# Performance work log

Hardware: AMD Instinct MI355X
Metric: run time of the kernel (lower is better)

Reference implementation:

```python
import jax, jax.numpy as jnp
import numpy as np

# Config (matches init_kwargs)
N, A, H, W = 4, 16, 384, 384
B_SIZE = 8      # block_size per spatial dim
STRIDE = 4      # block_stride per spatial dim (overlapping blocks)
THRESH = 2.0    # singular-value soft threshold
NB = (H - B_SIZE) // STRIDE + 1   # blocks per spatial dim (95)
P = B_SIZE * B_SIZE               # pixels per block (64)


def _block_indices():
    """Flat pixel index for each (block, in-block pixel): [NB*NB, P] int32."""
    starts = np.arange(NB) * STRIDE
    ih = starts[:, None] + np.arange(B_SIZE)              # [NB, b] row coords
    flat = ih[:, None, :, None] * W + ih[None, :, None, :]  # [NBh, NBw, b, b]
    return flat.reshape(NB * NB, P).astype(np.int32)


def setup_inputs() -> dict:
    key = jax.random.key(0)
    x = jax.random.normal(key, (N, A, H, W), dtype=jnp.float32)
    idx = jnp.asarray(_block_indices())
    # precompute_normalization: overlap-add of ones -> per-pixel block count
    block_weights = jnp.zeros(H * W, jnp.float32).at[idx].add(1.0).reshape(H, W)
    return {"x": x, "block_weights": block_weights}


def reference(x, block_weights):
    idx = jnp.asarray(_block_indices())           # [B, P]
    # self.shift = (0, 0) on the first forward call -> rolls are identity
    x = jnp.roll(x, (0, 0), axis=(-2, -1))
    xf = x.reshape(N, A, H * W)
    blocks = xf[:, :, idx]                        # [N, A, B, P] block extraction
    m = jnp.transpose(blocks, (0, 2, 3, 1))       # 'n a b p -> n b p a' -> [N,B,P,A]
    U, S, Vh = jnp.linalg.svd(m, full_matrices=False)  # U:[N,B,P,A] S:[N,B,A] Vh:[N,B,A,A]
    S = jnp.maximum(S - THRESH, 0.0)              # soft-threshold singular values
    m = (U * S[..., None, :]) @ Vh                # U diag(S) Vh, [N,B,P,A]
    blocks = jnp.transpose(m, (0, 3, 1, 2))       # 'n b p a -> n a b p'
    # adjoint: overlap-add fold, then normalize by block counts
    out = jnp.zeros((N, A, H * W), x.dtype).at[:, :, idx].add(blocks)
    out = out.reshape(N, A, H, W) / block_weights
    return jnp.roll(out, (0, 0), axis=(-2, -1))
```

## Files before the change

kernel.cpp:

```cpp
#include <hip/hip_runtime.h>


typedef __attribute__((ext_vector_type(2))) float v2f;
typedef __attribute__((ext_vector_type(4))) float f32x4;
typedef __attribute__((ext_vector_type(8))) short s16x8;
typedef union { float4 f4; v2f v2[2]; } f4v2;

#define N_      4
#define A_      16
#define H_      384
#define W_      384
#define PLANE_  (H_*W_)
#define NB_     95
#define NBB_    (NB_*NB_)
#define NMAT_   (N_*NBB_)
#define NWAVE_  ((NMAT_ + 3) / 4)
#define NSWEEP_ 4
#define PHI_BYTES_ ((size_t)NMAT_ * 256 * 4)

__device__ __forceinline__ v2f pk_fma(v2f a, v2f b, v2f c) {
    v2f d; asm("v_pk_fma_f32 %0, %1, %2, %3" : "=v"(d) : "v"(a), "v"(b), "v"(c));
    return d;
}
__device__ __forceinline__ v2f pk_mul(v2f a, v2f b) {
    v2f d; asm("v_pk_mul_f32 %0, %1, %2" : "=v"(d) : "v"(a), "v"(b));
    return d;
}

__device__ __forceinline__ unsigned cvtpk_bf16(float a, float b) {
    unsigned d;
    asm("v_cvt_pk_bf16_f32 %0, %1, %2" : "=v"(d) : "v"(a), "v"(b));
    return d;
}
__device__ __forceinline__ float asf_(unsigned u) {
    union { unsigned u; float f; } x; x.u = u; return x.f;
}
typedef union { s16x8 s8; unsigned u[4]; } frag8;

__device__ __forceinline__ void split8(const float4 A, const float4 B,
                                       frag8& hi, frag8& lo) {
    hi.u[0] = cvtpk_bf16(A.x, A.y);
    hi.u[1] = cvtpk_bf16(A.z, A.w);
    hi.u[2] = cvtpk_bf16(B.x, B.y);
    hi.u[3] = cvtpk_bf16(B.z, B.w);
    const float l0 = A.x - asf_(hi.u[0] << 16);
    const float l1 = A.y - asf_(hi.u[0] & 0xFFFF0000u);
    const float l2 = A.z - asf_(hi.u[1] << 16);
    const float l3 = A.w - asf_(hi.u[1] & 0xFFFF0000u);
    const float l4 = B.x - asf_(hi.u[2] << 16);
    const float l5 = B.y - asf_(hi.u[2] & 0xFFFF0000u);
    const float l6 = B.z - asf_(hi.u[3] << 16);
    const float l7 = B.w - asf_(hi.u[3] & 0xFFFF0000u);
    lo.u[0] = cvtpk_bf16(l0, l1);
    lo.u[1] = cvtpk_bf16(l2, l3);
    lo.u[2] = cvtpk_bf16(l4, l5);
    lo.u[3] = cvtpk_bf16(l6, l7);
}

template<int CTRL>
__device__ __forceinline__ float dpp16(float v) {
    union { float f; int i; } u; u.f = v;
    u.i = __builtin_amdgcn_mov_dpp(u.i, CTRL, 0xF, 0xF, true);
    return u.f;
}

#define QP1_ 0xB1
#define QP2_ 0x4E
#define QP3_ 0x1B
#define HM_  0x141
#define FM_  0x140
#define R8_  0x128

template<int M>
__device__ __forceinline__ float lane_xor16(float v) {
    if constexpr (M == 1)       return dpp16<QP1_>(v);
    else if constexpr (M == 2)  return dpp16<QP2_>(v);
    else if constexpr (M == 3)  return dpp16<QP3_>(v);
    else if constexpr (M == 7)  return dpp16<HM_>(v);
    else if constexpr (M == 8)  return dpp16<R8_>(v);
    else if constexpr (M == 15) return dpp16<FM_>(v);
    else {
        union { float f; int i; } u; u.f = v;
        u.i = __builtin_amdgcn_ds_swizzle(u.i, (M << 10) | 0x1F);
        return u.f;
    }
}

template<int M>
__device__ __forceinline__ void jacobi_round(v2f w[8], float& nrm, const int j) {
    v2f pw[8];
    #pragma unroll
    for (int i = 0; i < 8; ++i) {
        pw[i][0] = lane_xor16<M>(w[i][0]);
        pw[i][1] = lane_xor16<M>(w[i][1]);
    }
    const float pn = lane_xor16<M>(nrm);

    v2f d0 = w[0]*pw[0], d1 = w[1]*pw[1];
    #pragma unroll
    for (int i = 2; i < 8; i += 2) {
        d0 = __builtin_elementwise_fma(w[i],   pw[i],   d0);
        d1 = __builtin_elementwise_fma(w[i+1], pw[i+1], d1);
    }
    const v2f ds = d0 + d1;
    const float gam = ds[0] + ds[1];

    const bool  low = ((j ^ M) > j);
    const float na  = low ? nrm : pn;
    const float nb  = low ? pn  : nrm;

    const float thr = 1e-12f * (na + nb);
    const bool  rot = fabsf(gam) > thr;
    const float gs  = rot ? gam : 1.f;
    const float zeta = (nb - na) * (0.5f * __builtin_amdgcn_rcpf(gs));
    const float rt   = __builtin_amdgcn_rcpf(
                           fabsf(zeta) +
                           __builtin_amdgcn_sqrtf(__builtin_fmaf(zeta, zeta, 1.f)));
    float t  = copysignf(rt, zeta);
    float c  = __builtin_amdgcn_rsqf(__builtin_fmaf(t, t, 1.f));
    float sv = c * t;
    if (!rot) { c = 1.f; sv = 0.f; t = 0.f; }

    const float ss = low ? -sv : sv;
    const v2f c2 = {c, c}, sp = {ss, ss};
    #pragma unroll
    for (int i = 0; i < 8; ++i)
        w[i] = __builtin_elementwise_fma(c2, w[i], sp*pw[i]);

    nrm = __builtin_fmaf(low ? -t : t, gam, nrm);
}

__device__ __forceinline__ void gram_jacobi_phi(
        const float* __restrict__ x, const int wid, const int warp,
        const int lane, float Gl[4][4][320]) {
    const int g   = lane >> 4;
    const int j   = lane & 15;
    const int kq4 = g * 4;

    #pragma unroll
    for (int s = 0; s < 4; ++s) {
        const int id  = wid * 4 + s;
        const int n   = id / NBB_;
        const int rem = id % NBB_;
        const int bi  = rem / NB_;
        const int bj  = rem % NB_;
        const float* bp = x + (size_t)n * (A_ * PLANE_) + (size_t)j * PLANE_
                            + (bi*4 + g) * W_ + bj*4;

        const float4 va = *(const float4*)(bp);
        const float4 vb = *(const float4*)(bp + 4);
        const float4 vc = *(const float4*)(bp + 4*W_);
        const float4 vd = *(const float4*)(bp + 4*W_ + 4);

        frag8 hi0, lo0, hi1, lo1;
        split8(va, vb, hi0, lo0);
        split8(vc, vd, hi1, lo1);

        f32x4 C = {0.f, 0.f, 0.f, 0.f};
        C = __builtin_amdgcn_mfma_f32_16x16x32_bf16(lo0.s8, hi0.s8, C, 0, 0, 0);
        C = __builtin_amdgcn_mfma_f32_16x16x32_bf16(hi0.s8, lo0.s8, C, 0, 0, 0);
        C = __builtin_amdgcn_mfma_f32_16x16x32_bf16(hi0.s8, hi0.s8, C, 0, 0, 0);
        C = __builtin_amdgcn_mfma_f32_16x16x32_bf16(lo1.s8, hi1.s8, C, 0, 0, 0);
        C = __builtin_amdgcn_mfma_f32_16x16x32_bf16(hi1.s8, lo1.s8, C, 0, 0, 0);
        C = __builtin_amdgcn_mfma_f32_16x16x32_bf16(hi1.s8, hi1.s8, C, 0, 0, 0);

        *(float4*)&Gl[warp][s][j*20 + kq4] = make_float4(C[0], C[1], C[2], C[3]);
    }
    __builtin_amdgcn_wave_barrier();

    v2f w[8];
    {
        f4v2 t0, t1, t2, t3;
        t0.f4 = *(const float4*)&Gl[warp][g][j*20 + 0];
        t1.f4 = *(const float4*)&Gl[warp][g][j*20 + 4];
        t2.f4 = *(const float4*)&Gl[warp][g][j*20 + 8];
        t3.f4 = *(const float4*)&Gl[warp][g][j*20 + 12];
        w[0]=t0.v2[0]; w[1]=t0.v2[1]; w[2]=t1.v2[0]; w[3]=t1.v2[1];
        w[4]=t2.v2[0]; w[5]=t2.v2[1]; w[6]=t3.v2[0]; w[7]=t3.v2[1];
    }
    float nrm;
    {
        v2f d = pk_mul(w[0], w[0]);
        #pragma unroll
        for (int i = 1; i < 8; ++i) d = pk_fma(w[i], w[i], d);
        nrm = d[0] + d[1];
    }

    for (int sweep = 0; sweep < NSWEEP_; ++sweep) {
        jacobi_round<1>(w, nrm, j);  jacobi_round<2>(w, nrm, j);
        jacobi_round<3>(w, nrm, j);  jacobi_round<4>(w, nrm, j);
        jacobi_round<5>(w, nrm, j);  jacobi_round<6>(w, nrm, j);
        jacobi_round<7>(w, nrm, j);  jacobi_round<8>(w, nrm, j);
        jacobi_round<9>(w, nrm, j);  jacobi_round<10>(w, nrm, j);
        jacobi_round<11>(w, nrm, j); jacobi_round<12>(w, nrm, j);
        jacobi_round<13>(w, nrm, j); jacobi_round<14>(w, nrm, j);
        jacobi_round<15>(w, nrm, j);
    }
    {
        v2f d = pk_mul(w[0], w[0]);
        #pragma unroll
        for (int i = 1; i < 8; ++i) d = pk_fma(w[i], w[i], d);
        nrm = d[0] + d[1];
    }
    float rho = 0.f;
    if (nrm > 16.f) {
        const float lam = __builtin_amdgcn_sqrtf(nrm);
        rho = (1.f - 2.f * __builtin_amdgcn_rsqf(lam)) * __builtin_amdgcn_rcpf(nrm);
    }

    __builtin_amdgcn_wave_barrier();
    *(float4*)&Gl[warp][g][j*20 + 0]  = make_float4(w[0][0], w[0][1], w[1][0], w[1][1]);
    *(float4*)&Gl[warp][g][j*20 + 4]  = make_float4(w[2][0], w[2][1], w[3][0], w[3][1]);
    *(float4*)&Gl[warp][g][j*20 + 8]  = make_float4(w[4][0], w[4][1], w[5][0], w[5][1]);
    *(float4*)&Gl[warp][g][j*20 + 12] = make_float4(w[6][0], w[6][1], w[7][0], w[7][1]);
    Gl[warp][g][j*20 + 16] = rho;
    __builtin_amdgcn_wave_barrier();

    {
        const int kg = lane >> 4;
        const int mn = lane & 15;
        f32x4 PhiC[4];
        #pragma unroll
        for (int s = 0; s < 4; ++s) {
            frag8 Ahi, Alo, Bhi, Blo;
            if (kg < 2) {
                float av[8], bv[8];
                #pragma unroll
                for (int e = 0; e < 8; ++e) {
                    const int k = kg*8 + e;
                    const float wv = Gl[warp][s][k*20 + mn];
                    const float rh = Gl[warp][s][k*20 + 16];
                    bv[e] = wv;
                    av[e] = wv * rh;
                }
                split8(make_float4(av[0],av[1],av[2],av[3]),
                       make_float4(av[4],av[5],av[6],av[7]), Ahi, Alo);
                split8(make_float4(bv[0],bv[1],bv[2],bv[3]),
                       make_float4(bv[4],bv[5],bv[6],bv[7]), Bhi, Blo);
            } else {
                Ahi.u[0]=0u; Ahi.u[1]=0u; Ahi.u[2]=0u; Ahi.u[3]=0u;
                Alo = Ahi; Bhi = Ahi; Blo = Ahi;
            }
            f32x4 C = {0.f, 0.f, 0.f, 0.f};
            C = __builtin_amdgcn_mfma_f32_16x16x32_bf16(Alo.s8, Bhi.s8, C, 0, 0, 0);
            C = __builtin_amdgcn_mfma_f32_16x16x32_bf16(Ahi.s8, Blo.s8, C, 0, 0, 0);
            C = __builtin_amdgcn_mfma_f32_16x16x32_bf16(Ahi.s8, Bhi.s8, C, 0, 0, 0);
            PhiC[s] = C;
        }
        __builtin_amdgcn_wave_barrier();
        #pragma unroll
        for (int s = 0; s < 4; ++s) {
            #pragma unroll
            for (int r2 = 0; r2 < 4; ++r2)
                Gl[warp][s][(4*kg + r2)*20 + mn] = PhiC[s][r2];
        }
        __builtin_amdgcn_wave_barrier();
    }
}

__global__ __launch_bounds__(256, 8)
void llr_phi(const float* __restrict__ x, float* __restrict__ phiG) {
    __shared__ __align__(16) float Gl[4][4][320];
    const int warp = threadIdx.x >> 6;
    const int lane = threadIdx.x & 63;

    const int xcd = blockIdx.x & 7, idx = blockIdx.x >> 3;
    const int wg  = (xcd == 0 ? idx : 283 + (xcd - 1) * 282 + idx);
    const int wid = wg * 4 + warp;
    if (wid >= NWAVE_) return;

    gram_jacobi_phi(x, wid, warp, lane, Gl);

    const int g = lane >> 4, j = lane & 15;
    float* pb = phiG + (size_t)(wid*4 + g) * 256 + j * 16;
    const float4 p0 = *(const float4*)&Gl[warp][g][j*20 + 0];
    const float4 p1 = *(const float4*)&Gl[warp][g][j*20 + 4];
    const float4 p2 = *(const float4*)&Gl[warp][g][j*20 + 8];
    const float4 p3 = *(const float4*)&Gl[warp][g][j*20 + 12];
    *(float4*)&pb[0]  = p0;  *(float4*)&pb[4]  = p1;
    *(float4*)&pb[8]  = p2;  *(float4*)&pb[12] = p3;
}

__global__ __launch_bounds__(256, 8)
void llr_out2(const float* __restrict__ x, const float* __restrict__ phiG,
              float* __restrict__ out) {
    __shared__ __align__(16) float Sl[16][260];

    const int b  = (blockIdx.x & 7) * 288 + (blockIdx.x >> 3);
    const int n  = b / 576;
    const int tt = b % 576;
    const int tr = tt / 12, tc = tt % 12;
    const int r0 = tr*8, c0 = tc*32;
    const int cr0 = tr*2, cc0 = tc*8;

    const int r = threadIdx.x >> 5;
    const int c = threadIdx.x & 31;
    const int lcc = ((r >> 2) << 3) + (c >> 2);
    const size_t sb = (size_t)n * (A_*PLANE_) + (size_t)(r0 + r) * W_ + (c0 + c);

    {
        const int lc = threadIdx.x >> 4;
        const int fo = (threadIdx.x & 15) * 4;
        const int ci = cr0 + (lc >> 3);
        const int cj = cc0 + (lc & 7);
        const int bi0 = max(ci - 1, 0), bi1 = min(ci, NB_ - 1);
        const int bj0 = max(cj - 1, 0), bj1 = min(cj, NB_ - 1);
        const size_t r00 = ((size_t)(n*NBB_ + bi0*NB_ + bj0))*256;
        const size_t r01 = ((size_t)(n*NBB_ + bi0*NB_ + bj1))*256;
        const size_t r10 = ((size_t)(n*NBB_ + bi1*NB_ + bj0))*256;
        const size_t r11 = ((size_t)(n*NBB_ + bi1*NB_ + bj1))*256;
        #pragma unroll
        for (int it = 0; it < 4; ++it) {
            const int off = fo + it*64;
            const float4 a  = *(const float4*)&phiG[r00 + off];
            const float4 bq = *(const float4*)&phiG[r01 + off];
            const float4 cq = *(const float4*)&phiG[r10 + off];
            const float4 d  = *(const float4*)&phiG[r11 + off];
            float4 s;
            s.x = (a.x + bq.x + cq.x + d.x) * 0.25f;
            s.y = (a.y + bq.y + cq.y + d.y) * 0.25f;
            s.z = (a.z + bq.z + cq.z + d.z) * 0.25f;
            s.w = (a.w + bq.w + cq.w + d.w) * 0.25f;
            *(float4*)&Sl[lc][off] = s;
        }
    }

    float xk[16];
    #pragma unroll
    for (int k = 0; k < 16; ++k) xk[k] = x[sb + (size_t)k * PLANE_];

    __syncthreads();

    v2f acc[8];
    #pragma unroll
    for (int i = 0; i < 8; ++i) acc[i] = (v2f){0.f, 0.f};
    #pragma unroll
    for (int k = 0; k < 16; ++k) {
        const v2f xv = {xk[k], xk[k]};
        f4v2 s0, s1, s2, s3;
        s0.f4 = *(const float4*)&Sl[lcc][k*16 + 0];
        s1.f4 = *(const float4*)&Sl[lcc][k*16 + 4];
        s2.f4 = *(const float4*)&Sl[lcc][k*16 + 8];
        s3.f4 = *(const float4*)&Sl[lcc][k*16 + 12];
        acc[0] = pk_fma(xv, s0.v2[0], acc[0]);
        acc[1] = pk_fma(xv, s0.v2[1], acc[1]);
        acc[2] = pk_fma(xv, s1.v2[0], acc[2]);
        acc[3] = pk_fma(xv, s1.v2[1], acc[3]);
        acc[4] = pk_fma(xv, s2.v2[0], acc[4]);
        acc[5] = pk_fma(xv, s2.v2[1], acc[5]);
        acc[6] = pk_fma(xv, s3.v2[0], acc[6]);
        acc[7] = pk_fma(xv, s3.v2[1], acc[7]);
    }
    #pragma unroll
    for (int i = 0; i < 8; ++i) {
        out[sb + (size_t)(2*i)     * PLANE_] = acc[i][0];
        out[sb + (size_t)(2*i + 1) * PLANE_] = acc[i][1];
    }
}

__global__ __launch_bounds__(256, 5)
void llr_fused(const float* __restrict__ x, float* __restrict__ out) {
    __shared__ __align__(16) float Gl[4][4][320];
    const int warp = threadIdx.x >> 6;
    const int lane = threadIdx.x & 63;
    const int wid  = blockIdx.x * 4 + warp;
    if (wid >= NWAVE_) return;

    gram_jacobi_phi(x, wid, warp, lane, Gl);

    const int pr = lane >> 3, pc = lane & 7;
    for (int s = 0; s < 4; ++s) {
        const int id = wid*4 + s;
        const int n = id / NBB_, rem = id % NBB_;
        const int bi = rem / NB_, bj = rem % NB_;
        const int base = n*(A_*PLANE_) + (bi*4+pr)*W_ + (bj*4+pc);
        float mr[16];
        #pragma unroll
        for (int a = 0; a < 16; ++a) mr[a] = x[base + a*PLANE_];
        float o[16];
        #pragma unroll
        for (int a = 0; a < 16; ++a) o[a] = 0.f;
        #pragma unroll
        for (int k = 0; k < 16; ++k) {
            const float mk = mr[k];
            const float4 f0 = *(const float4*)&Gl[warp][s][k*20 + 0];
            const float4 f1 = *(const float4*)&Gl[warp][s][k*20 + 4];
            const float4 f2 = *(const float4*)&Gl[warp][s][k*20 + 8];
            const float4 f3 = *(const float4*)&Gl[warp][s][k*20 + 12];
            o[0]+=mk*f0.x;  o[1]+=mk*f0.y;  o[2]+=mk*f0.z;  o[3]+=mk*f0.w;
            o[4]+=mk*f1.x;  o[5]+=mk*f1.y;  o[6]+=mk*f1.z;  o[7]+=mk*f1.w;
            o[8]+=mk*f2.x;  o[9]+=mk*f2.y;  o[10]+=mk*f2.z; o[11]+=mk*f2.w;
            o[12]+=mk*f3.x; o[13]+=mk*f3.y; o[14]+=mk*f3.z; o[15]+=mk*f3.w;
        }
        #pragma unroll
        for (int a = 0; a < 16; ++a)
            unsafeAtomicAdd(&out[base + a*PLANE_], o[a]);
    }
}

__global__ __launch_bounds__(256)
void llr_div(float* __restrict__ out, const float* __restrict__ bw) {
    const int i = (blockIdx.x * 256 + threadIdx.x) * 4;
    float4 o = *(float4*)&out[i];
    const float4 bv = *(const float4*)&bw[i % PLANE_];
    o.x /= bv.x; o.y /= bv.y; o.z /= bv.z; o.w /= bv.w;
    *(float4*)&out[i] = o;
}

extern "C" void kernel_launch(void* const* d_in, const int* in_sizes, int n_in,
                              void* d_out, int out_size, void* d_ws, size_t ws_size,
                              hipStream_t stream) {
    (void)in_sizes; (void)n_in;
    const float* x  = (const float*)d_in[0];
    const float* bw = (const float*)d_in[1];
    float* out = (float*)d_out;

    if (ws_size >= PHI_BYTES_) {
        float* phiG = (float*)d_ws;
        hipLaunchKernelGGL(llr_phi,  dim3((NWAVE_ + 3) / 4), dim3(256), 0, stream, x, phiG);
        hipLaunchKernelGGL(llr_out2, dim3(4 * 48 * 12),      dim3(256), 0, stream, x, phiG, out);
    } else {
        hipMemsetAsync(out, 0, (size_t)out_size * sizeof(float), stream);
        hipLaunchKernelGGL(llr_fused, dim3((NWAVE_ + 3) / 4), dim3(256), 0, stream, x, out);
        hipLaunchKernelGGL(llr_div, dim3((N_*A_*PLANE_) / (256*4)), dim3(256), 0, stream, out, bw);
    }
}
```

Before: 172.8 us.

## Process eight matrices per wave with two interleaved Jacobi chains

```diff
diff --git a/kernel.cpp b/kernel.cpp
--- a/kernel.cpp
+++ b/kernel.cpp
@@ -14,7 +14,7 @@
 #define NB_     95
 #define NBB_    (NB_*NB_)
 #define NMAT_   (N_*NBB_)
-#define NWAVE_  ((NMAT_ + 3) / 4)
+#define NWAVE8_ ((NMAT_ + 7) / 8)
 #define NSWEEP_ 4
 #define PHI_BYTES_ ((size_t)NMAT_ * 256 * 4)
 
@@ -87,141 +87,205 @@
 }
 
 template<int M>
-__device__ __forceinline__ void jacobi_round(v2f w[8], float& nrm, const int j) {
-    v2f pw[8];
+__device__ __forceinline__ void jacobi_round2(v2f wA[8], v2f wB[8],
+                                              float& nrmA, float& nrmB,
+                                              const int j) {
+    v2f pA[8], pB[8];
     #pragma unroll
     for (int i = 0; i < 8; ++i) {
-        pw[i][0] = lane_xor16<M>(w[i][0]);
-        pw[i][1] = lane_xor16<M>(w[i][1]);
-    }
-    const float pn = lane_xor16<M>(nrm);
-
-    v2f d0 = w[0]*pw[0], d1 = w[1]*pw[1];
+        pA[i][0] = lane_xor16<M>(wA[i][0]);
+        pA[i][1] = lane_xor16<M>(wA[i][1]);
+        pB[i][0] = lane_xor16<M>(wB[i][0]);
+        pB[i][1] = lane_xor16<M>(wB[i][1]);
+    }
+    const float pnA = lane_xor16<M>(nrmA);
+    const float pnB = lane_xor16<M>(nrmB);
+
+    v2f a0 = wA[0]*pA[0], a1 = wA[1]*pA[1];
+    v2f b0 = wB[0]*pB[0], b1 = wB[1]*pB[1];
     #pragma unroll
     for (int i = 2; i < 8; i += 2) {
-        d0 = __builtin_elementwise_fma(w[i],   pw[i],   d0);
-        d1 = __builtin_elementwise_fma(w[i+1], pw[i+1], d1);
-    }
-    const v2f ds = d0 + d1;
-    const float gam = ds[0] + ds[1];
-
-    const bool  low = ((j ^ M) > j);
-    const float na  = low ? nrm : pn;
-    const float nb  = low ? pn  : nrm;
-
-    const float thr = 1e-12f * (na + nb);
-    const bool  rot = fabsf(gam) > thr;
-    const float gs  = rot ? gam : 1.f;
-    const float zeta = (nb - na) * (0.5f * __builtin_amdgcn_rcpf(gs));
-    const float rt   = __builtin_amdgcn_rcpf(
-                           fabsf(zeta) +
-                           __builtin_amdgcn_sqrtf(__builtin_fmaf(zeta, zeta, 1.f)));
-    float t  = copysignf(rt, zeta);
-    float c  = __builtin_amdgcn_rsqf(__builtin_fmaf(t, t, 1.f));
-    float sv = c * t;
-    if (!rot) { c = 1.f; sv = 0.f; t = 0.f; }
-
-    const float ss = low ? -sv : sv;
-    const v2f c2 = {c, c}, sp = {ss, ss};
-    #pragma unroll
-    for (int i = 0; i < 8; ++i)
-        w[i] = __builtin_elementwise_fma(c2, w[i], sp*pw[i]);
-
-    nrm = __builtin_fmaf(low ? -t : t, gam, nrm);
+        a0 = __builtin_elementwise_fma(wA[i],   pA[i],   a0);
+        a1 = __builtin_elementwise_fma(wA[i+1], pA[i+1], a1);
+        b0 = __builtin_elementwise_fma(wB[i],   pB[i],   b0);
+        b1 = __builtin_elementwise_fma(wB[i+1], pB[i+1], b1);
+    }
+    const v2f dsA = a0 + a1;
+    const v2f dsB = b0 + b1;
+    const float gamA = dsA[0] + dsA[1];
+    const float gamB = dsB[0] + dsB[1];
+
+    const bool low = ((j ^ M) > j);
+
+    const float naA = low ? nrmA : pnA;
+    const float nbA = low ? pnA  : nrmA;
+    const float thrA = 1e-12f * (naA + nbA);
+    const bool  rotA = fabsf(gamA) > thrA;
+    const float gsA  = rotA ? gamA : 1.f;
+    const float zA = (nbA - naA) * (0.5f * __builtin_amdgcn_rcpf(gsA));
+    const float rtA = __builtin_amdgcn_rcpf(
+                          fabsf(zA) +
+                          __builtin_amdgcn_sqrtf(__builtin_fmaf(zA, zA, 1.f)));
+    float tA = copysignf(rtA, zA);
+    float cA = __builtin_amdgcn_rsqf(__builtin_fmaf(tA, tA, 1.f));
+    float svA = cA * tA;
+    if (!rotA) { cA = 1.f; svA = 0.f; tA = 0.f; }
+
+    const float naB = low ? nrmB : pnB;
+    const float nbB = low ? pnB  : nrmB;
+    const float thrB = 1e-12f * (naB + nbB);
+    const bool  rotB = fabsf(gamB) > thrB;
+    const float gsB  = rotB ? gamB : 1.f;
+    const float zB = (nbB - naB) * (0.5f * __builtin_amdgcn_rcpf(gsB));
+    const float rtB = __builtin_amdgcn_rcpf(
+                          fabsf(zB) +
+                          __builtin_amdgcn_sqrtf(__builtin_fmaf(zB, zB, 1.f)));
+    float tB = copysignf(rtB, zB);
+    float cB = __builtin_amdgcn_rsqf(__builtin_fmaf(tB, tB, 1.f));
+    float svB = cB * tB;
+    if (!rotB) { cB = 1.f; svB = 0.f; tB = 0.f; }
+
+    const float ssA = low ? -svA : svA;
+    const float ssB = low ? -svB : svB;
+    const v2f cA2 = {cA, cA}, sA2 = {ssA, ssA};
+    const v2f cB2 = {cB, cB}, sB2 = {ssB, ssB};
+    #pragma unroll
+    for (int i = 0; i < 8; ++i) {
+        wA[i] = __builtin_elementwise_fma(cA2, wA[i], sA2*pA[i]);
+        wB[i] = __builtin_elementwise_fma(cB2, wB[i], sB2*pB[i]);
+    }
+
+    nrmA = __builtin_fmaf(low ? -tA : tA, gamA, nrmA);
+    nrmB = __builtin_fmaf(low ? -tB : tB, gamB, nrmB);
 }
 
 __device__ __forceinline__ void gram_jacobi_phi(
         const float* __restrict__ x, const int wid, const int warp,
-        const int lane, float Gl[4][4][320]) {
+        const int lane, float Gl[4][8][320]) {
     const int g   = lane >> 4;
     const int j   = lane & 15;
     const int kq4 = g * 4;
 
     #pragma unroll
-    for (int s = 0; s < 4; ++s) {
-        const int id  = wid * 4 + s;
-        const int n   = id / NBB_;
-        const int rem = id % NBB_;
-        const int bi  = rem / NB_;
-        const int bj  = rem % NB_;
-        const float* bp = x + (size_t)n * (A_ * PLANE_) + (size_t)j * PLANE_
-                            + (bi*4 + g) * W_ + bj*4;
-
-        const float4 va = *(const float4*)(bp);
-        const float4 vb = *(const float4*)(bp + 4);
-        const float4 vc = *(const float4*)(bp + 4*W_);
-        const float4 vd = *(const float4*)(bp + 4*W_ + 4);
-
-        frag8 hi0, lo0, hi1, lo1;
-        split8(va, vb, hi0, lo0);
-        split8(vc, vd, hi1, lo1);
-
-        f32x4 C = {0.f, 0.f, 0.f, 0.f};
-        C = __builtin_amdgcn_mfma_f32_16x16x32_bf16(lo0.s8, hi0.s8, C, 0, 0, 0);
-        C = __builtin_amdgcn_mfma_f32_16x16x32_bf16(hi0.s8, lo0.s8, C, 0, 0, 0);
-        C = __builtin_amdgcn_mfma_f32_16x16x32_bf16(hi0.s8, hi0.s8, C, 0, 0, 0);
-        C = __builtin_amdgcn_mfma_f32_16x16x32_bf16(lo1.s8, hi1.s8, C, 0, 0, 0);
-        C = __builtin_amdgcn_mfma_f32_16x16x32_bf16(hi1.s8, lo1.s8, C, 0, 0, 0);
-        C = __builtin_amdgcn_mfma_f32_16x16x32_bf16(hi1.s8, hi1.s8, C, 0, 0, 0);
-
-        *(float4*)&Gl[warp][s][j*20 + kq4] = make_float4(C[0], C[1], C[2], C[3]);
+    for (int s = 0; s < 8; ++s) {
+        const int id = wid * 8 + s;
+        if (id < NMAT_) {
+            const int n   = id / NBB_;
+            const int rem = id % NBB_;
+            const int bi  = rem / NB_;
+            const int bj  = rem % NB_;
+            const float* bp = x + (size_t)n * (A_ * PLANE_) + (size_t)j * PLANE_
+                                + (bi*4 + g) * W_ + bj*4;
+
+            const float4 va = *(const float4*)(bp);
+            const float4 vb = *(const float4*)(bp + 4);
+            const float4 vc = *(const float4*)(bp + 4*W_);
+            const float4 vd = *(const float4*)(bp + 4*W_ + 4);
+
+            frag8 hi0, lo0, hi1, lo1;
+            split8(va, vb, hi0, lo0);
+            split8(vc, vd, hi1, lo1);
+
+            f32x4 C = {0.f, 0.f, 0.f, 0.f};
+            C = __builtin_amdgcn_mfma_f32_16x16x32_bf16(lo0.s8, hi0.s8, C, 0, 0, 0);
+            C = __builtin_amdgcn_mfma_f32_16x16x32_bf16(hi0.s8, lo0.s8, C, 0, 0, 0);
+            C = __builtin_amdgcn_mfma_f32_16x16x32_bf16(hi0.s8, hi0.s8, C, 0, 0, 0);
+            C = __builtin_amdgcn_mfma_f32_16x16x32_bf16(lo1.s8, hi1.s8, C, 0, 0, 0);
+            C = __builtin_amdgcn_mfma_f32_16x16x32_bf16(hi1.s8, lo1.s8, C, 0, 0, 0);
+            C = __builtin_amdgcn_mfma_f32_16x16x32_bf16(hi1.s8, hi1.s8, C, 0, 0, 0);
+
+            *(float4*)&Gl[warp][s][j*20 + kq4] = make_float4(C[0], C[1], C[2], C[3]);
+        } else {
+            *(float4*)&Gl[warp][s][j*20 + kq4] = make_float4(0.f, 0.f, 0.f, 0.f);
+        }
     }
     __builtin_amdgcn_wave_barrier();
 
-    v2f w[8];
+    v2f wA[8], wB[8];
     {
         f4v2 t0, t1, t2, t3;
         t0.f4 = *(const float4*)&Gl[warp][g][j*20 + 0];
         t1.f4 = *(const float4*)&Gl[warp][g][j*20 + 4];
         t2.f4 = *(const float4*)&Gl[warp][g][j*20 + 8];
         t3.f4 = *(const float4*)&Gl[warp][g][j*20 + 12];
-        w[0]=t0.v2[0]; w[1]=t0.v2[1]; w[2]=t1.v2[0]; w[3]=t1.v2[1];
-        w[4]=t2.v2[0]; w[5]=t2.v2[1]; w[6]=t3.v2[0]; w[7]=t3.v2[1];
-    }
-    float nrm;
+        wA[0]=t0.v2[0]; wA[1]=t0.v2[1]; wA[2]=t1.v2[0]; wA[3]=t1.v2[1];
+        wA[4]=t2.v2[0]; wA[5]=t2.v2[1]; wA[6]=t3.v2[0]; wA[7]=t3.v2[1];
+        t0.f4 = *(const float4*)&Gl[warp][g+4][j*20 + 0];
+        t1.f4 = *(const float4*)&Gl[warp][g+4][j*20 + 4];
+        t2.f4 = *(const float4*)&Gl[warp][g+4][j*20 + 8];
+        t3.f4 = *(const float4*)&Gl[warp][g+4][j*20 + 12];
+        wB[0]=t0.v2[0]; wB[1]=t0.v2[1]; wB[2]=t1.v2[0]; wB[3]=t1.v2[1];
+        wB[4]=t2.v2[0]; wB[5]=t2.v2[1]; wB[6]=t3.v2[0]; wB[7]=t3.v2[1];
+    }
+    float nrmA, nrmB;
     {
-        v2f d = pk_mul(w[0], w[0]);
-        #pragma unroll
-        for (int i = 1; i < 8; ++i) d = pk_fma(w[i], w[i], d);
-        nrm = d[0] + d[1];
+        v2f dA = pk_mul(wA[0], wA[0]);
+        v2f dB = pk_mul(wB[0], wB[0]);
+        #pragma unroll
+        for (int i = 1; i < 8; ++i) {
+            dA = pk_fma(wA[i], wA[i], dA);
+            dB = pk_fma(wB[i], wB[i], dB);
+        }
+        nrmA = dA[0] + dA[1];
+        nrmB = dB[0] + dB[1];
     }
 
     for (int sweep = 0; sweep < NSWEEP_; ++sweep) {
-        jacobi_round<1>(w, nrm, j);  jacobi_round<2>(w, nrm, j);
-        jacobi_round<3>(w, nrm, j);  jacobi_round<4>(w, nrm, j);
-        jacobi_round<5>(w, nrm, j);  jacobi_round<6>(w, nrm, j);
-        jacobi_round<7>(w, nrm, j);  jacobi_round<8>(w, nrm, j);
-        jacobi_round<9>(w, nrm, j);  jacobi_round<10>(w, nrm, j);
-        jacobi_round<11>(w, nrm, j); jacobi_round<12>(w, nrm, j);
-        jacobi_round<13>(w, nrm, j); jacobi_round<14>(w, nrm, j);
-        jacobi_round<15>(w, nrm, j);
+        jacobi_round2<1>(wA, wB, nrmA, nrmB, j);
+        jacobi_round2<2>(wA, wB, nrmA, nrmB, j);
+        jacobi_round2<3>(wA, wB, nrmA, nrmB, j);
+        jacobi_round2<4>(wA, wB, nrmA, nrmB, j);
+        jacobi_round2<5>(wA, wB, nrmA, nrmB, j);
+        jacobi_round2<6>(wA, wB, nrmA, nrmB, j);
+        jacobi_round2<7>(wA, wB, nrmA, nrmB, j);
+        jacobi_round2<8>(wA, wB, nrmA, nrmB, j);
+        jacobi_round2<9>(wA, wB, nrmA, nrmB, j);
+        jacobi_round2<10>(wA, wB, nrmA, nrmB, j);
+        jacobi_round2<11>(wA, wB, nrmA, nrmB, j);
+        jacobi_round2<12>(wA, wB, nrmA, nrmB, j);
+        jacobi_round2<13>(wA, wB, nrmA, nrmB, j);
+        jacobi_round2<14>(wA, wB, nrmA, nrmB, j);
+        jacobi_round2<15>(wA, wB, nrmA, nrmB, j);
     }
     {
-        v2f d = pk_mul(w[0], w[0]);
-        #pragma unroll
-        for (int i = 1; i < 8; ++i) d = pk_fma(w[i], w[i], d);
-        nrm = d[0] + d[1];
-    }
-    float rho = 0.f;
-    if (nrm > 16.f) {
-        const float lam = __builtin_amdgcn_sqrtf(nrm);
-        rho = (1.f - 2.f * __builtin_amdgcn_rsqf(lam)) * __builtin_amdgcn_rcpf(nrm);
+        v2f dA = pk_mul(wA[0], wA[0]);
+        v2f dB = pk_mul(wB[0], wB[0]);
+        #pragma unroll
+        for (int i = 1; i < 8; ++i) {
+            dA = pk_fma(wA[i], wA[i], dA);
+            dB = pk_fma(wB[i], wB[i], dB);
+        }
+        nrmA = dA[0] + dA[1];
+        nrmB = dB[0] + dB[1];
+    }
+    float rhoA = 0.f, rhoB = 0.f;
+    if (nrmA > 16.f) {
+        const float lam = __builtin_amdgcn_sqrtf(nrmA);
+        rhoA = (1.f - 2.f * __builtin_amdgcn_rsqf(lam)) * __builtin_amdgcn_rcpf(nrmA);
+    }
+    if (nrmB > 16.f) {
+        const float lam = __builtin_amdgcn_sqrtf(nrmB);
+        rhoB = (1.f - 2.f * __builtin_amdgcn_rsqf(lam)) * __builtin_amdgcn_rcpf(nrmB);
     }
 
     __builtin_amdgcn_wave_barrier();
-    *(float4*)&Gl[warp][g][j*20 + 0]  = make_float4(w[0][0], w[0][1], w[1][0], w[1][1]);
-    *(float4*)&Gl[warp][g][j*20 + 4]  = make_float4(w[2][0], w[2][1], w[3][0], w[3][1]);
-    *(float4*)&Gl[warp][g][j*20 + 8]  = make_float4(w[4][0], w[4][1], w[5][0], w[5][1]);
-    *(float4*)&Gl[warp][g][j*20 + 12] = make_float4(w[6][0], w[6][1], w[7][0], w[7][1]);
-    Gl[warp][g][j*20 + 16] = rho;
+    *(float4*)&Gl[warp][g][j*20 + 0]  = make_float4(wA[0][0], wA[0][1], wA[1][0], wA[1][1]);
+    *(float4*)&Gl[warp][g][j*20 + 4]  = make_float4(wA[2][0], wA[2][1], wA[3][0], wA[3][1]);
+    *(float4*)&Gl[warp][g][j*20 + 8]  = make_float4(wA[4][0], wA[4][1], wA[5][0], wA[5][1]);
+    *(float4*)&Gl[warp][g][j*20 + 12] = make_float4(wA[6][0], wA[6][1], wA[7][0], wA[7][1]);
+    Gl[warp][g][j*20 + 16] = rhoA;
+    *(float4*)&Gl[warp][g+4][j*20 + 0]  = make_float4(wB[0][0], wB[0][1], wB[1][0], wB[1][1]);
+    *(float4*)&Gl[warp][g+4][j*20 + 4]  = make_float4(wB[2][0], wB[2][1], wB[3][0], wB[3][1]);
+    *(float4*)&Gl[warp][g+4][j*20 + 8]  = make_float4(wB[4][0], wB[4][1], wB[5][0], wB[5][1]);
+    *(float4*)&Gl[warp][g+4][j*20 + 12] = make_float4(wB[6][0], wB[6][1], wB[7][0], wB[7][1]);
+    Gl[warp][g+4][j*20 + 16] = rhoB;
     __builtin_amdgcn_wave_barrier();
 
     {
         const int kg = lane >> 4;
         const int mn = lane & 15;
-        f32x4 PhiC[4];
-        #pragma unroll
-        for (int s = 0; s < 4; ++s) {
+        #pragma unroll
+        for (int s = 0; s < 8; ++s) {
             frag8 Ahi, Alo, Bhi, Blo;
             if (kg < 2) {
                 float av[8], bv[8];
@@ -245,40 +309,43 @@
             C = __builtin_amdgcn_mfma_f32_16x16x32_bf16(Alo.s8, Bhi.s8, C, 0, 0, 0);
             C = __builtin_amdgcn_mfma_f32_16x16x32_bf16(Ahi.s8, Blo.s8, C, 0, 0, 0);
             C = __builtin_amdgcn_mfma_f32_16x16x32_bf16(Ahi.s8, Bhi.s8, C, 0, 0, 0);
-            PhiC[s] = C;
-        }
-        __builtin_amdgcn_wave_barrier();
-        #pragma unroll
-        for (int s = 0; s < 4; ++s) {
+            __builtin_amdgcn_wave_barrier();
             #pragma unroll
             for (int r2 = 0; r2 < 4; ++r2)
-                Gl[warp][s][(4*kg + r2)*20 + mn] = PhiC[s][r2];
-        }
-        __builtin_amdgcn_wave_barrier();
-    }
-}
-
-__global__ __launch_bounds__(256, 8)
+                Gl[warp][s][(4*kg + r2)*20 + mn] = C[r2];
+            __builtin_amdgcn_wave_barrier();
+        }
+    }
+}
+
+__global__ __launch_bounds__(256, 4)
 void llr_phi(const float* __restrict__ x, float* __restrict__ phiG) {
-    __shared__ __align__(16) float Gl[4][4][320];
+    __shared__ __align__(16) float Gl[4][8][320];
     const int warp = threadIdx.x >> 6;
     const int lane = threadIdx.x & 63;
 
     const int xcd = blockIdx.x & 7, idx = blockIdx.x >> 3;
-    const int wg  = (xcd == 0 ? idx : 283 + (xcd - 1) * 282 + idx);
+    const int wg  = (xcd == 0 ? idx : 142 + (xcd - 1) * 141 + idx);
     const int wid = wg * 4 + warp;
-    if (wid >= NWAVE_) return;
+    if (wid >= NWAVE8_) return;
 
     gram_jacobi_phi(x, wid, warp, lane, Gl);
 
     const int g = lane >> 4, j = lane & 15;
-    float* pb = phiG + (size_t)(wid*4 + g) * 256 + j * 16;
-    const float4 p0 = *(const float4*)&Gl[warp][g][j*20 + 0];
-    const float4 p1 = *(const float4*)&Gl[warp][g][j*20 + 4];
-    const float4 p2 = *(const float4*)&Gl[warp][g][j*20 + 8];
-    const float4 p3 = *(const float4*)&Gl[warp][g][j*20 + 12];
-    *(float4*)&pb[0]  = p0;  *(float4*)&pb[4]  = p1;
-    *(float4*)&pb[8]  = p2;  *(float4*)&pb[12] = p3;
+    #pragma unroll
+    for (int h = 0; h < 2; ++h) {
+        const int s  = g + 4*h;
+        const int id = wid*8 + s;
+        if (id < NMAT_) {
+            float* pb = phiG + (size_t)id * 256 + j * 16;
+            const float4 p0 = *(const float4*)&Gl[warp][s][j*20 + 0];
+            const float4 p1 = *(const float4*)&Gl[warp][s][j*20 + 4];
+            const float4 p2 = *(const float4*)&Gl[warp][s][j*20 + 8];
+            const float4 p3 = *(const float4*)&Gl[warp][s][j*20 + 12];
+            *(float4*)&pb[0]  = p0;  *(float4*)&pb[4]  = p1;
+            *(float4*)&pb[8]  = p2;  *(float4*)&pb[12] = p3;
+        }
+    }
 }
 
 __global__ __launch_bounds__(256, 8)
@@ -358,19 +425,20 @@
     }
 }
 
-__global__ __launch_bounds__(256, 5)
+__global__ __launch_bounds__(256, 4)
 void llr_fused(const float* __restrict__ x, float* __restrict__ out) {
-    __shared__ __align__(16) float Gl[4][4][320];
+    __shared__ __align__(16) float Gl[4][8][320];
     const int warp = threadIdx.x >> 6;
     const int lane = threadIdx.x & 63;
     const int wid  = blockIdx.x * 4 + warp;
-    if (wid >= NWAVE_) return;
+    if (wid >= NWAVE8_) return;
 
     gram_jacobi_phi(x, wid, warp, lane, Gl);
 
     const int pr = lane >> 3, pc = lane & 7;
-    for (int s = 0; s < 4; ++s) {
-        const int id = wid*4 + s;
+    for (int s = 0; s < 8; ++s) {
+        const int id = wid*8 + s;
+        if (id >= NMAT_) break;
         const int n = id / NBB_, rem = id % NBB_;
         const int bi = rem / NB_, bj = rem % NB_;
         const int base = n*(A_*PLANE_) + (bi*4+pr)*W_ + (bj*4+pc);
@@ -417,11 +485,11 @@
 
     if (ws_size >= PHI_BYTES_) {
         float* phiG = (float*)d_ws;
-        hipLaunchKernelGGL(llr_phi,  dim3((NWAVE_ + 3) / 4), dim3(256), 0, stream, x, phiG);
-        hipLaunchKernelGGL(llr_out2, dim3(4 * 48 * 12),      dim3(256), 0, stream, x, phiG, out);
+        hipLaunchKernelGGL(llr_phi,  dim3((NWAVE8_ + 3) / 4), dim3(256), 0, stream, x, phiG);
+        hipLaunchKernelGGL(llr_out2, dim3(4 * 48 * 12),       dim3(256), 0, stream, x, phiG, out);
     } else {
         hipMemsetAsync(out, 0, (size_t)out_size * sizeof(float), stream);
-        hipLaunchKernelGGL(llr_fused, dim3((NWAVE_ + 3) / 4), dim3(256), 0, stream, x, out);
+        hipLaunchKernelGGL(llr_fused, dim3((NWAVE8_ + 3) / 4), dim3(256), 0, stream, x, out);
         hipLaunchKernelGGL(llr_div, dim3((N_*A_*PLANE_) / (256*4)), dim3(256), 0, stream, out, bw);
     }
 }
```

Result: slower. 193.1 us (+11.8%).
